# Optimization experiments

Hardware: AMD Instinct MI355X
Metric: run time of the kernel (lower is better)

## Reference

```python
import jax, jax.numpy as jnp
import numpy as np
from jax import lax

USER_NUM = 100000
COMP_NUM = 50000
ENTITY_NUM = USER_NUM + COMP_NUM + 2  # 150002
N_ACTIVE = USER_NUM + COMP_NUM        # 150000 valid graph nodes
REL_NUM = 200
D = 128
T = 12        # timesteps
E = 250000    # edges per timestep
S = 20000     # seed (LSTM-updated) nodes per timestep
B = 1024      # user batch
USER_ID_MAX = 99999


def setup_inputs() -> dict:
    key = jax.random.key(0)
    ks = jax.random.split(key, 16)
    ent_emb = jax.random.normal(ks[0], (ENTITY_NUM, D), jnp.float32) * 0.02
    c0_emb = jax.random.normal(ks[1], (ENTITY_NUM, D), jnp.float32) * 0.02
    rel_emb = jax.random.normal(ks[2], (REL_NUM, D), jnp.float32) * 0.02
    W_ih = jax.random.normal(ks[3], (4 * D, D), jnp.float32) * (1.0 / np.sqrt(D))
    W_hh = jax.random.normal(ks[4], (4 * D, D), jnp.float32) * (1.0 / np.sqrt(D))
    b_ih = jax.random.normal(ks[5], (4 * D,), jnp.float32) * 0.01
    b_hh = jax.random.normal(ks[6], (4 * D,), jnp.float32) * 0.01
    src = jax.random.randint(ks[7], (T, E), 0, N_ACTIVE, jnp.int32)
    dst = jax.random.randint(ks[8], (T, E), 0, N_ACTIVE, jnp.int32)
    rel_idx = jax.random.randint(ks[9], (T, E), 0, REL_NUM, jnp.int32)
    # unique seed nodes per timestep (scatter targets must not collide)
    seed_keys = jax.random.split(ks[10], T)
    seed_idx = jax.vmap(lambda k: jax.random.permutation(k, N_ACTIVE)[:S])(seed_keys).astype(jnp.int32)
    user_batch = jax.random.randint(ks[11], (B,), 0, USER_NUM, jnp.int32)
    comp_target = jax.random.randint(ks[12], (B,), 0, COMP_NUM, jnp.int32)
    job_target = jax.random.randint(ks[13], (B,), 0, REL_NUM // 2, jnp.int32)
    return {"ent_emb": ent_emb, "c0_emb": c0_emb, "rel_emb": rel_emb,
            "W_ih": W_ih, "W_hh": W_hh, "b_ih": b_ih, "b_hh": b_hh,
            "src": src, "dst": dst, "rel_idx": rel_idx, "seed_idx": seed_idx,
            "user_batch": user_batch, "comp_target": comp_target, "job_target": job_target}


def reference(ent_emb, c0_emb, rel_emb, W_ih, W_hh, b_ih, b_hh,
              src, dst, rel_idx, seed_idx, user_batch, comp_target, job_target):
    def step(carry, xs):
        h, c = carry                       # [N, D] node_emb / cx
        s, d, r, seed = xs
        # msg_GCN: m = src_node_emb * rel_emb[rel]; reduce_GCN: mean over mailbox
        m = h[s] * rel_emb[r]              # [E, D]
        msum = jax.ops.segment_sum(m, d, num_segments=ENTITY_NUM)
        cnt = jax.ops.segment_sum(jnp.ones((E,), h.dtype), d, num_segments=ENTITY_NUM)
        x = h + msum / jnp.maximum(cnt, 1.0)[:, None]   # update_node: node_emb + node_emb2
        # LSTMCell on seed nodes only (input = aggregated emb, state = pre-agg emb, cx)
        xi, hp, cp = x[seed], h[seed], c[seed]          # [S, D]
        gates = xi @ W_ih.T + b_ih + hp @ W_hh.T + b_hh  # [S, 4D]
        ig, fg, gg, og = jnp.split(gates, 4, axis=-1)
        cn = jax.nn.sigmoid(fg) * cp + jax.nn.sigmoid(ig) * jnp.tanh(gg)
        hn = jax.nn.sigmoid(og) * jnp.tanh(cn)
        return (x.at[seed].set(hn), c.at[seed].set(cn)), None

    (h, _c), _ = lax.scan(step, (ent_emb, c0_emb), (src, dst, rel_idx, seed_idx))

    u = h[user_batch]                                   # [B, D] user time embeddings
    # company softmax-CE (logsumexp over all companies)
    tc = ent_emb[comp_target + USER_ID_MAX + 1]
    all_c = ent_emb[USER_ID_MAX + 1: USER_ID_MAX + 1 + COMP_NUM]  # [COMP_NUM, D]
    pos_c = jnp.sum(u * tc, axis=1)
    comp_loss = -jnp.sum(pos_c - jax.nn.logsumexp(u @ all_c.T, axis=1))
    # job (relation) softmax-CE over rel_num // 2 jobs
    tj = rel_emb[job_target]
    all_j = rel_emb[: REL_NUM // 2]
    pos_j = jnp.sum(u * tj, axis=1)
    job_loss = -jnp.sum(pos_j - jax.nn.logsumexp(u @ all_j.T, axis=1))
    return jnp.stack([comp_loss, job_loss])
```

## Files before the change

kernel.cpp:

```cpp
#include <hip/hip_runtime.h>
#include <math.h>

typedef __attribute__((ext_vector_type(8))) short short8;
typedef __attribute__((ext_vector_type(8))) unsigned short u16x8;
typedef __attribute__((ext_vector_type(4))) float f32x4;

#define USER_NUM_  100000
#define COMP_NUM_  50000
#define EN         150002
#define REL_NUM_   200
#define DD         128
#define TT         12
#define EE         250000
#define SS         20000
#define BB         1024
#define NBLK       587
#define PPART      125
#define TILES_PP   25
#define NB         37
#define BSH        12
#define CHUNK      4096
#define NCH        62

__device__ inline unsigned short f2bf(float f) {
    unsigned u = __float_as_uint(f);
    unsigned r = (u + 0x7fffu + ((u >> 16) & 1u)) >> 16;
    return (unsigned short)r;
}

__device__ inline float bf2f(unsigned short u) {
    return __uint_as_float((unsigned)u << 16);
}

__device__ inline float sigmoidf_(float x) { return 1.f / (1.f + __expf(-x)); }

__device__ inline void lse_push(float v, float& m, float& s) {
    if (v <= m) { s += __expf(v - m); }
    else { s = s * __expf(m - v) + 1.f; m = v; }
}

__device__ inline void lse_merge(float& M, float& S, float M2, float S2) {
    float Mn = fmaxf(M, M2);
    S = S * __expf(M - Mn) + S2 * __expf(M2 - Mn);
    M = Mn;
}

__global__ __launch_bounds__(256) void packBF_k(const float* __restrict__ src, ushort4* __restrict__ dst, int n4) {
    int i = blockIdx.x * 256 + threadIdx.x;
    if (i >= n4) return;
    float4 v = ((const float4*)src)[i];
    ushort4 o;
    o.x = f2bf(v.x); o.y = f2bf(v.y); o.z = f2bf(v.z); o.w = f2bf(v.w);
    dst[i] = o;
}

__global__ __launch_bounds__(256) void zero_i32_k(int* __restrict__ p, int n) {
    int i = blockIdx.x * 256 + threadIdx.x;
    if (i < n) p[i] = 0;
}

__global__ __launch_bounds__(256) void prepW_k(const float* __restrict__ Wih, const float* __restrict__ Whh,
                                               const float* __restrict__ bih, const float* __restrict__ bhh,
                                               short* __restrict__ Wt, float* __restrict__ bsum) {
    int n = blockIdx.x;
    int k = threadIdx.x;
    float v = (k < 128) ? Wih[n * 128 + k] : Whh[n * 128 + (k - 128)];
    Wt[n * 256 + k] = (short)f2bf(v);
    if (k == 0) bsum[n] = bih[n] + bhh[n];
}

__global__ __launch_bounds__(256) void binA_k(const int* __restrict__ dst, int* __restrict__ bcnt,
                                              int t0) {
    int slot = blockIdx.y;
    int tid = threadIdx.x;
    int e = blockIdx.x * 256 + tid;
    __shared__ int lcnt[NB];
    if (tid < NB) lcnt[tid] = 0;
    __syncthreads();
    if (e < EE) {
        int d = __builtin_nontemporal_load(&dst[(size_t)(t0 + slot) * EE + e]);
        atomicAdd(&lcnt[d >> BSH], 1);
    }
    __syncthreads();
    if (tid < NB && lcnt[tid] > 0) atomicAdd(&bcnt[slot * NB + tid], lcnt[tid]);
}

__global__ __launch_bounds__(64) void binScan_k(const int* __restrict__ bcnt, int* __restrict__ bbase,
                                                int* __restrict__ bcur, int nt) {
    int slot = threadIdx.x;
    if (slot >= nt) return;
    int b = 0;
    for (int c = 0; c < NB; ++c) {
        bbase[slot * (NB + 1) + c] = b;
        bcur[slot * NB + c] = b;
        b += bcnt[slot * NB + c];
    }
    bbase[slot * (NB + 1) + NB] = b;
}

__global__ __launch_bounds__(256) void binB_k(const int* __restrict__ src, const int* __restrict__ dst,
                                              const int* __restrict__ rel, int* __restrict__ bcur,
                                              int2* __restrict__ bucketed, int t0) {
    int slot = blockIdx.y;
    int tid = threadIdx.x;
    int c0 = blockIdx.x * CHUNK;
    __shared__ int lcnt[NB], lbase[NB], gbase[NB], lcur[NB];
    __shared__ int2 stage[CHUNK];
    if (tid < NB) lcnt[tid] = 0;
    __syncthreads();

    int myb[16]; int2 myv[16];
#pragma unroll
    for (int i = 0; i < 16; ++i) {
        int e = c0 + i * 256 + tid;
        if (e < EE) {
            size_t gi = (size_t)(t0 + slot) * EE + e;
            int d = __builtin_nontemporal_load(&dst[gi]);
            int s = __builtin_nontemporal_load(&src[gi]);
            int r = __builtin_nontemporal_load(&rel[gi]);
            myb[i] = d >> BSH;
            myv[i] = make_int2(d, s | (r << 18));
            atomicAdd(&lcnt[myb[i]], 1);
        } else myb[i] = -1;
    }
    __syncthreads();
    if (tid == 0) {
        int b = 0;
        for (int c = 0; c < NB; ++c) { lbase[c] = b; b += lcnt[c]; }
    }
    __syncthreads();
    if (tid < NB) {
        gbase[tid] = (lcnt[tid] > 0) ? atomicAdd(&bcur[slot * NB + tid], lcnt[tid]) : 0;
        lcur[tid] = lbase[tid];
    }
    __syncthreads();
#pragma unroll
    for (int i = 0; i < 16; ++i) {
        if (myb[i] >= 0) {
            int p = atomicAdd(&lcur[myb[i]], 1);
            stage[p] = myv[i];
        }
    }
    __syncthreads();
    int w = tid >> 6, lane = tid & 63;
    int2* bout = bucketed + (size_t)slot * EE;
    for (int b = w; b < NB; b += 4) {
        int cnt = lcnt[b], lb = lbase[b], gb = gbase[b];
        for (int j = lane; j < cnt; j += 64)
            bout[gb + j] = stage[lb + j];
    }
}

__global__ __launch_bounds__(256) void histB_k(const int2* __restrict__ bucketed,
                                               const int* __restrict__ bbase,
                                               int* __restrict__ startp) {
    int b = blockIdx.x, slot = blockIdx.y;
    int tid = threadIdx.x;
    int base_ent = b << BSH;
    int nloc = EN - base_ent; if (nloc > 4096) nloc = 4096;
    __shared__ int lcnt[4096];
    for (int i = tid; i < nloc; i += 256) lcnt[i] = 0;
    __syncthreads();
    int e0 = bbase[slot * (NB + 1) + b], e1 = bbase[slot * (NB + 1) + b + 1];
    for (int e = e0 + tid; e < e1; e += 256) {
        int2 ed = bucketed[(size_t)slot * EE + e];
        atomicAdd(&lcnt[ed.x - base_ent], 1);
    }
    __syncthreads();
    for (int i = tid; i < nloc; i += 256) startp[(size_t)slot * EN + base_ent + i] = lcnt[i];
}

__global__ __launch_bounds__(256) void scanA_k(int* __restrict__ startp, int* __restrict__ bsums) {
    int slot = blockIdx.y;
    int tid = threadIdx.x;
    int i = blockIdx.x * 256 + tid;
    int v = (i < EN) ? startp[slot * EN + i] : 0;
    __shared__ int lds[256];
    lds[tid] = v; __syncthreads();
#pragma unroll
    for (int o = 1; o < 256; o <<= 1) {
        int x = (tid >= o) ? lds[tid - o] : 0;
        __syncthreads();
        lds[tid] += x;
        __syncthreads();
    }
    if (i < EN) startp[slot * EN + i] = lds[tid] - v;
    if (tid == 255) bsums[slot * NBLK + blockIdx.x] = lds[tid];
}

__global__ __launch_bounds__(1024) void scanB_k(int* __restrict__ bsums) {
    int slot = blockIdx.x;
    int tid = threadIdx.x;
    int v = (tid < NBLK) ? bsums[slot * NBLK + tid] : 0;
    __shared__ int lds[1024];
    lds[tid] = v; __syncthreads();
#pragma unroll
    for (int o = 1; o < 1024; o <<= 1) {
        int x = (tid >= o) ? lds[tid - o] : 0;
        __syncthreads();
        lds[tid] += x;
        __syncthreads();
    }
    if (tid < NBLK) bsums[slot * NBLK + tid] = lds[tid] - v;
}

__global__ __launch_bounds__(256) void scanC_k(int* __restrict__ startp, const int* __restrict__ bsums) {
    int slot = blockIdx.y;
    int i = blockIdx.x * 256 + threadIdx.x;
    if (i < EN) startp[slot * EN + i] += bsums[slot * NBLK + blockIdx.x];
}

__global__ __launch_bounds__(256) void scatB_k(const int2* __restrict__ bucketed,
                                               const int* __restrict__ bbase,
                                               int* __restrict__ startp, int* __restrict__ pairs) {
    int b = blockIdx.x, slot = blockIdx.y;
    int tid = threadIdx.x;
    int base_ent = b << BSH;
    int nloc = EN - base_ent; if (nloc > 4096) nloc = 4096;
    __shared__ int lcur[4096];
    for (int i = tid; i < nloc; i += 256) lcur[i] = startp[(size_t)slot * EN + base_ent + i];
    __syncthreads();
    int e0 = bbase[slot * (NB + 1) + b], e1 = bbase[slot * (NB + 1) + b + 1];
    for (int e = e0 + tid; e < e1; e += 256) {
        int2 ed = bucketed[(size_t)slot * EE + e];
        int pos = atomicAdd(&lcur[ed.x - base_ent], 1);
        pairs[(size_t)slot * EE + pos] = ed.y;
    }
    __syncthreads();
    for (int i = tid; i < nloc; i += 256) startp[(size_t)slot * EN + base_ent + i] = lcur[i];
}

__global__ __launch_bounds__(256) void agg_k(const unsigned short* __restrict__ hold,
                                             unsigned short* __restrict__ hnew,
                                             const unsigned short* __restrict__ Rbf,
                                             const int* __restrict__ endp_all,
                                             const int* __restrict__ pairs, int slot) {
    int tid = threadIdx.x;
    int d = blockIdx.x * 16 + (tid >> 4);
    int l = tid & 15;
    if (d >= EN) return;
    const int* endp = endp_all + (size_t)slot * EN;
    int e0 = (d > 0) ? endp[d - 1] : 0;
    int e1 = endp[d];
    const int* pp = pairs + (size_t)slot * EE;
    float acc[8];
#pragma unroll
    for (int j = 0; j < 8; ++j) acc[j] = 0.f;
    int e = e0;
    for (; e + 2 <= e1; e += 2) {
        int pk0 = pp[e], pk1 = pp[e + 1];
        u16x8 h0 = *(const u16x8*)(hold + (size_t)(pk0 & 0x3FFFF) * DD + l * 8);
        u16x8 r0 = *(const u16x8*)(Rbf + (size_t)(pk0 >> 18) * DD + l * 8);
        u16x8 h1 = *(const u16x8*)(hold + (size_t)(pk1 & 0x3FFFF) * DD + l * 8);
        u16x8 r1 = *(const u16x8*)(Rbf + (size_t)(pk1 >> 18) * DD + l * 8);
#pragma unroll
        for (int j = 0; j < 8; ++j)
            acc[j] = fmaf(bf2f(h1[j]), bf2f(r1[j]), fmaf(bf2f(h0[j]), bf2f(r0[j]), acc[j]));
    }
    if (e < e1) {
        int pk0 = pp[e];
        u16x8 h0 = *(const u16x8*)(hold + (size_t)(pk0 & 0x3FFFF) * DD + l * 8);
        u16x8 r0 = *(const u16x8*)(Rbf + (size_t)(pk0 >> 18) * DD + l * 8);
#pragma unroll
        for (int j = 0; j < 8; ++j)
            acc[j] = fmaf(bf2f(h0[j]), bf2f(r0[j]), acc[j]);
    }
    u16x8 hd = *(const u16x8*)(hold + (size_t)d * DD + l * 8);
    int c = e1 - e0;
    float inv = (c > 0) ? 1.f / (float)c : 0.f;
    u16x8 o;
#pragma unroll
    for (int j = 0; j < 8; ++j) o[j] = f2bf(fmaf(acc[j], inv, bf2f(hd[j])));
    *(u16x8*)(hnew + (size_t)d * DD + l * 8) = o;
}

__global__ __launch_bounds__(256) void lstm_k(const unsigned short* __restrict__ hold,
                                              unsigned short* __restrict__ hnew,
                                              unsigned short* __restrict__ cbuf, const short* __restrict__ Wt,
                                              const float* __restrict__ bsum, const int* __restrict__ seed) {
    int w = threadIdx.x >> 6;
    int lane = threadIdx.x & 63;
    int lrow = lane & 15, lhi = lane >> 4;
    int m0 = blockIdx.x * 32;
    int w32 = w * 32;

    const unsigned short* pxi[2];
    const unsigned short* php[2];
#pragma unroll
    for (int mi = 0; mi < 2; ++mi) {
        int m = m0 + mi * 16 + lrow;
        int sd = seed[m];
        pxi[mi] = hnew + (size_t)sd * DD;
        php[mi] = hold + (size_t)sd * DD;
    }

    f32x4 acc[2][4][2];
#pragma unroll
    for (int mi = 0; mi < 2; ++mi)
#pragma unroll
        for (int g = 0; g < 4; ++g)
#pragma unroll
            for (int s = 0; s < 2; ++s)
                acc[mi][g][s] = (f32x4){0.f, 0.f, 0.f, 0.f};

#pragma unroll
    for (int kk = 0; kk < 8; ++kk) {
        int klane = kk * 32 + lhi * 8;
        short8 af[2];
#pragma unroll
        for (int mi = 0; mi < 2; ++mi) {
            const unsigned short* p = (klane < 128) ? (pxi[mi] + klane) : (php[mi] + (klane - 128));
            af[mi] = *(const short8*)p;
        }
#pragma unroll
        for (int g = 0; g < 4; ++g)
#pragma unroll
            for (int s = 0; s < 2; ++s) {
                int col = g * 128 + w32 + s * 16 + lrow;
                short8 bf = *(const short8*)(Wt + col * 256 + klane);
                acc[0][g][s] = __builtin_amdgcn_mfma_f32_16x16x32_bf16(af[0], bf, acc[0][g][s], 0, 0, 0);
                acc[1][g][s] = __builtin_amdgcn_mfma_f32_16x16x32_bf16(af[1], bf, acc[1][g][s], 0, 0, 0);
            }
    }

    __syncthreads();

#pragma unroll
    for (int mi = 0; mi < 2; ++mi) {
#pragma unroll
        for (int r = 0; r < 4; ++r) {
            int m = m0 + mi * 16 + lhi * 4 + r;
            int sd = seed[m];
#pragma unroll
            for (int s = 0; s < 2; ++s) {
                int d = w32 + s * 16 + lrow;
                float ig = acc[mi][0][s][r] + bsum[d];
                float fg = acc[mi][1][s][r] + bsum[128 + d];
                float gg = acc[mi][2][s][r] + bsum[256 + d];
                float og = acc[mi][3][s][r] + bsum[384 + d];
                float cp = bf2f(cbuf[(size_t)sd * DD + d]);
                float cn = sigmoidf_(fg) * cp + sigmoidf_(ig) * tanhf(gg);
                float hn = sigmoidf_(og) * tanhf(cn);
                cbuf[(size_t)sd * DD + d] = f2bf(cn);
                hnew[(size_t)sd * DD + d] = f2bf(hn);
            }
        }
    }
}

__global__ __launch_bounds__(256) void packU_k(const unsigned short* __restrict__ hfin, const int* __restrict__ ub,
                                               short* __restrict__ Ubf) {
    int i = blockIdx.x * 256 + threadIdx.x;
    if (i >= BB * DD) return;
    int u = i >> 7, k = i & 127;
    Ubf[i] = (short)hfin[(size_t)ub[u] * DD + k];
}

__global__ __launch_bounds__(256) void comp_mfma_k(const short* __restrict__ Ubf, const short* __restrict__ Cbf,
                                                   float* __restrict__ partm, float* __restrict__ parts) {
    int w = threadIdx.x >> 6, lane = threadIdx.x & 63;
    int lrow = lane & 15, lhi = lane >> 4;
    int ubase = blockIdx.x * 128 + w * 32;
    int p = blockIdx.y;

    short8 a[2][4];
#pragma unroll
    for (int s2 = 0; s2 < 2; ++s2)
#pragma unroll
        for (int kc = 0; kc < 4; ++kc)
            a[s2][kc] = *(const short8*)(Ubf + (size_t)(ubase + s2 * 16 + lrow) * DD + kc * 32 + lhi * 8);

    float m[2][4], s[2][4];
#pragma unroll
    for (int s2 = 0; s2 < 2; ++s2)
#pragma unroll
        for (int r = 0; r < 4; ++r) { m[s2][r] = -1e30f; s[s2][r] = 0.f; }

    int c0 = p * TILES_PP * 16;
    for (int tile = 0; tile < TILES_PP; ++tile) {
        int comp = c0 + tile * 16 + lrow;
        f32x4 acc0 = {0.f, 0.f, 0.f, 0.f};
        f32x4 acc1 = {0.f, 0.f, 0.f, 0.f};
#pragma unroll
        for (int kc = 0; kc < 4; ++kc) {
            short8 b = *(const short8*)(Cbf + (size_t)comp * DD + kc * 32 + lhi * 8);
            acc0 = __builtin_amdgcn_mfma_f32_16x16x32_bf16(a[0][kc], b, acc0, 0, 0, 0);
            acc1 = __builtin_amdgcn_mfma_f32_16x16x32_bf16(a[1][kc], b, acc1, 0, 0, 0);
        }
#pragma unroll
        for (int r = 0; r < 4; ++r) {
            lse_push(acc0[r], m[0][r], s[0][r]);
            lse_push(acc1[r], m[1][r], s[1][r]);
        }
    }

#pragma unroll
    for (int s2 = 0; s2 < 2; ++s2)
#pragma unroll
        for (int r = 0; r < 4; ++r) {
            float M = m[s2][r], S = s[s2][r];
#pragma unroll
            for (int o = 1; o < 16; o <<= 1) {
                float M2 = __shfl_xor(M, o, 64);
                float S2 = __shfl_xor(S, o, 64);
                if (M2 > M) { S = S * __expf(M - M2) + S2; M = M2; }
                else { S += S2 * __expf(M2 - M); }
            }
            if (lrow == 0) {
                int u = ubase + s2 * 16 + lhi * 4 + r;
                partm[(size_t)u * PPART + p] = M;
                parts[(size_t)u * PPART + p] = S;
            }
        }
}

__global__ __launch_bounds__(256) void finish2_k(const unsigned short* __restrict__ hfin,
                                                 const float* __restrict__ ent,
                                                 const float* __restrict__ rel, const int* __restrict__ ub,
                                                 const int* __restrict__ ct, const int* __restrict__ jt,
                                                 const float* __restrict__ partm, const float* __restrict__ parts,
                                                 float* __restrict__ out) {
    __shared__ float s_u[4][128];
    int w = threadIdx.x >> 6, lane = threadIdx.x & 63;
    int u = blockIdx.x * 4 + w;

    const unsigned short* up = hfin + (size_t)ub[u] * DD;
    float u0 = bf2f(up[lane]), u1 = bf2f(up[lane + 64]);
    s_u[w][lane] = u0;
    s_u[w][lane + 64] = u1;

    const float* tcp = ent + (size_t)(USER_NUM_ + ct[u]) * DD;
    float pc = u0 * tcp[lane] + u1 * tcp[lane + 64];
    const float* tjp = rel + (size_t)jt[u] * DD;
    float pj = u0 * tjp[lane] + u1 * tjp[lane + 64];
#pragma unroll
    for (int o = 1; o < 64; o <<= 1) {
        pc += __shfl_xor(pc, o, 64);
        pj += __shfl_xor(pj, o, 64);
    }

    float M = partm[(size_t)u * PPART + lane];
    float S = parts[(size_t)u * PPART + lane];
    if (lane + 64 < PPART)
        lse_merge(M, S, partm[(size_t)u * PPART + lane + 64], parts[(size_t)u * PPART + lane + 64]);
#pragma unroll
    for (int o = 1; o < 64; o <<= 1) {
        float M2 = __shfl_xor(M, o, 64);
        float S2 = __shfl_xor(S, o, 64);
        lse_merge(M, S, M2, S2);
    }
    float lse_c = M + logf(S);

    int j1 = lane, j2 = lane + 64;
    bool v2 = j2 < (REL_NUM_ / 2);
    const float* r1 = rel + (size_t)j1 * DD;
    const float* r2 = rel + (size_t)(v2 ? j2 : 0) * DD;
    float d1 = 0.f, d2 = 0.f;
#pragma unroll 16
    for (int k = 0; k < DD; ++k) {
        float uk = s_u[w][k];
        d1 = fmaf(uk, r1[k], d1);
        d2 = fmaf(uk, r2[k], d2);
    }
    float Mj = d1, Sj = 1.f;
    if (v2) lse_push(d2, Mj, Sj);
#pragma unroll
    for (int o = 1; o < 64; o <<= 1) {
        float M2 = __shfl_xor(Mj, o, 64);
        float S2 = __shfl_xor(Sj, o, 64);
        lse_merge(Mj, Sj, M2, S2);
    }
    float lse_j = Mj + logf(Sj);

    if (lane == 0) {
        atomicAdd(&out[0], lse_c - pc);
        atomicAdd(&out[1], lse_j - pj);
    }
}

static inline size_t rup(size_t x) { return (x + 255) & ~(size_t)255; }

extern "C" void kernel_launch(void* const* d_in, const int* in_sizes, int n_in,
                              void* d_out, int out_size, void* d_ws, size_t ws_size,
                              hipStream_t stream) {
    const float* ent_emb = (const float*)d_in[0];
    const float* c0_emb  = (const float*)d_in[1];
    const float* rel_emb = (const float*)d_in[2];
    const float* W_ih    = (const float*)d_in[3];
    const float* W_hh    = (const float*)d_in[4];
    const float* b_ih    = (const float*)d_in[5];
    const float* b_hh    = (const float*)d_in[6];
    const int* src       = (const int*)d_in[7];
    const int* dst       = (const int*)d_in[8];
    const int* rel_idx   = (const int*)d_in[9];
    const int* seed_idx  = (const int*)d_in[10];
    const int* ubatch    = (const int*)d_in[11];
    const int* ctarg     = (const int*)d_in[12];
    const int* jtarg     = (const int*)d_in[13];
    float* out = (float*)d_out;

    const size_t HBH = (size_t)EN * DD * 2;

    char* base = (char*)d_ws;
    unsigned short* h0   = (unsigned short*)base;
    unsigned short* h1   = (unsigned short*)(base + HBH);
    unsigned short* cbuf = (unsigned short*)(base + 2 * HBH);

    int* startp; int* pairs; int* bsums; int2* bucketed; int* bcnt; int* bbase; int* bcur;
    short* Wt; float* bsumv; unsigned short* Rbf;
    auto place = [&](int NT) -> size_t {
        size_t o = 3 * HBH;
        startp   = (int*)(base + o);  o += rup((size_t)NT * EN * 4);
        pairs    = (int*)(base + o);  o += rup((size_t)NT * EE * 4);
        bucketed = (int2*)(base + o); o += rup((size_t)NT * EE * 8);
        bsums    = (int*)(base + o);  o += rup((size_t)NT * NBLK * 4);
        bcnt     = (int*)(base + o);  o += rup((size_t)NT * NB * 4);
        bbase    = (int*)(base + o);  o += rup((size_t)NT * (NB + 1) * 4);
        bcur     = (int*)(base + o);  o += rup((size_t)NT * NB * 4);
        Wt       = (short*)(base + o); o += rup(512 * 256 * 2);
        bsumv    = (float*)(base + o); o += rup(512 * 4);
        Rbf      = (unsigned short*)(base + o); o += rup((size_t)REL_NUM_ * DD * 2);
        return o;
    };

    const int cands[6] = {12, 6, 4, 3, 2, 1};
    int NT = 1;
    for (int i = 0; i < 6; ++i) {
        if (place(cands[i]) <= ws_size) { NT = cands[i]; break; }
    }
    place(NT);

    char* q = (char*)cbuf;
    short* Cbf = (short*)q;            q += rup((size_t)COMP_NUM_ * DD * 2);
    short* Ubf = (short*)q;            q += rup((size_t)BB * DD * 2);
    float* partm = (float*)q;          q += rup((size_t)BB * PPART * 4);
    float* parts = (float*)q;

    hipMemsetAsync(d_out, 0, 2 * sizeof(float), stream);

    const int n4 = EN * DD / 4;
    const int gcpy = (n4 + 255) / 256;
    const int ge = (EE + 255) / 256;

    prepW_k<<<512, 256, 0, stream>>>(W_ih, W_hh, b_ih, b_hh, Wt, bsumv);
    packBF_k<<<gcpy, 256, 0, stream>>>(ent_emb, (ushort4*)h0, n4);
    packBF_k<<<gcpy, 256, 0, stream>>>(c0_emb, (ushort4*)cbuf, n4);
    packBF_k<<<(REL_NUM_ * DD / 4 + 255) / 256, 256, 0, stream>>>(rel_emb, (ushort4*)Rbf, REL_NUM_ * DD / 4);

    auto build = [&](int t0, int nt) {
        zero_i32_k<<<(nt * NB + 255) / 256, 256, 0, stream>>>(bcnt, nt * NB);
        binA_k<<<dim3(ge, nt), 256, 0, stream>>>(dst, bcnt, t0);
        binScan_k<<<1, 64, 0, stream>>>(bcnt, bbase, bcur, nt);
        binB_k<<<dim3(NCH, nt), 256, 0, stream>>>(src, dst, rel_idx, bcur, bucketed, t0);
        histB_k<<<dim3(NB, nt), 256, 0, stream>>>(bucketed, bbase, startp);
        scanA_k<<<dim3(NBLK, nt), 256, 0, stream>>>(startp, bsums);
        scanB_k<<<nt, 1024, 0, stream>>>(bsums);
        scanC_k<<<dim3(NBLK, nt), 256, 0, stream>>>(startp, bsums);
        scatB_k<<<dim3(NB, nt), 256, 0, stream>>>(bucketed, bbase, startp, pairs);
    };

    unsigned short* hold = h0;
    unsigned short* hnew = h1;
    const int gagg = (EN + 15) / 16;

    for (int b0 = 0; b0 < TT; b0 += NT) {
        int nb = (TT - b0 < NT) ? (TT - b0) : NT;
        build(b0, nb);
        for (int k = 0; k < nb; ++k) {
            int t = b0 + k;
            agg_k<<<gagg, 256, 0, stream>>>(hold, hnew, Rbf, startp, pairs, k);
            lstm_k<<<SS / 32, 256, 0, stream>>>(hold, hnew, cbuf, Wt, bsumv, seed_idx + (size_t)t * SS);
            unsigned short* tmp = hold; hold = hnew; hnew = tmp;
        }
    }

    packBF_k<<<(COMP_NUM_ * DD / 4 + 255) / 256, 256, 0, stream>>>(ent_emb + (size_t)USER_NUM_ * DD,
                                                                   (ushort4*)Cbf, COMP_NUM_ * DD / 4);
    packU_k<<<(BB * DD + 255) / 256, 256, 0, stream>>>(hold, ubatch, Ubf);
    comp_mfma_k<<<dim3(BB / 128, PPART), 256, 0, stream>>>(Ubf, Cbf, partm, parts);
    finish2_k<<<BB / 4, 256, 0, stream>>>(hold, ent_emb, rel_emb, ubatch, ctarg, jtarg,
                                          partm, parts, out);
}
```

Measured before the change: 1.002 ms.

## Coarsen bin counting, stage company tiles in LDS, drop max-tracking in logsumexp

```diff
diff --git a/kernel.cpp b/kernel.cpp
--- a/kernel.cpp
+++ b/kernel.cpp
@@ -73,16 +73,22 @@
                                               int t0) {
     int slot = blockIdx.y;
     int tid = threadIdx.x;
-    int e = blockIdx.x * 256 + tid;
-    __shared__ int lcnt[NB];
-    if (tid < NB) lcnt[tid] = 0;
-    __syncthreads();
-    if (e < EE) {
-        int d = __builtin_nontemporal_load(&dst[(size_t)(t0 + slot) * EE + e]);
-        atomicAdd(&lcnt[d >> BSH], 1);
-    }
-    __syncthreads();
-    if (tid < NB && lcnt[tid] > 0) atomicAdd(&bcnt[slot * NB + tid], lcnt[tid]);
+    int c0 = blockIdx.x * CHUNK;
+    int w = tid >> 6;
+    __shared__ int lcnt[4][NB];
+    for (int i = tid; i < 4 * NB; i += 256) ((int*)lcnt)[i] = 0;
+    __syncthreads();
+#pragma unroll
+    for (int i = 0; i < 16; ++i) {
+        int e = c0 + i * 256 + tid;
+        if (e < EE) {
+            int d = __builtin_nontemporal_load(&dst[(size_t)(t0 + slot) * EE + e]);
+            atomicAdd(&lcnt[w][d >> BSH], 1);
+        }
+    }
+    __syncthreads();
+    if (tid < NB)
+        atomicAdd(&bcnt[slot * NB + tid], lcnt[0][tid] + lcnt[1][tid] + lcnt[2][tid] + lcnt[3][tid]);
 }
 
 __global__ __launch_bounds__(64) void binScan_k(const int* __restrict__ bcnt, int* __restrict__ bbase,
@@ -358,11 +364,14 @@
 
 __global__ __launch_bounds__(256) void comp_mfma_k(const short* __restrict__ Ubf, const short* __restrict__ Cbf,
                                                    float* __restrict__ partm, float* __restrict__ parts) {
-    int w = threadIdx.x >> 6, lane = threadIdx.x & 63;
+    int tid = threadIdx.x;
+    int w = tid >> 6, lane = tid & 63;
     int lrow = lane & 15, lhi = lane >> 4;
     int ubase = blockIdx.x * 128 + w * 32;
     int p = blockIdx.y;
 
+    __shared__ __align__(16) short ct[2][16][136];
+
     short8 a[2][4];
 #pragma unroll
     for (int s2 = 0; s2 < 2; ++s2)
@@ -370,27 +379,40 @@
         for (int kc = 0; kc < 4; ++kc)
             a[s2][kc] = *(const short8*)(Ubf + (size_t)(ubase + s2 * 16 + lrow) * DD + kc * 32 + lhi * 8);
 
-    float m[2][4], s[2][4];
+    float s[2][4];
 #pragma unroll
     for (int s2 = 0; s2 < 2; ++s2)
 #pragma unroll
-        for (int r = 0; r < 4; ++r) { m[s2][r] = -1e30f; s[s2][r] = 0.f; }
+        for (int r = 0; r < 4; ++r) s[s2][r] = 0.f;
 
     int c0 = p * TILES_PP * 16;
+    int srow = tid >> 4, scol = (tid & 15) * 8;
+    {
+        short8 v = *(const short8*)(Cbf + (size_t)(c0 + srow) * DD + scol);
+        *(short8*)&ct[0][srow][scol] = v;
+    }
+
     for (int tile = 0; tile < TILES_PP; ++tile) {
-        int comp = c0 + tile * 16 + lrow;
+        int cur = tile & 1;
+        short8 pf;
+        bool hn = (tile + 1 < TILES_PP);
+        if (hn)
+            pf = *(const short8*)(Cbf + (size_t)(c0 + (tile + 1) * 16 + srow) * DD + scol);
+        __syncthreads();
+        if (hn) *(short8*)&ct[cur ^ 1][srow][scol] = pf;
+
         f32x4 acc0 = {0.f, 0.f, 0.f, 0.f};
         f32x4 acc1 = {0.f, 0.f, 0.f, 0.f};
 #pragma unroll
         for (int kc = 0; kc < 4; ++kc) {
-            short8 b = *(const short8*)(Cbf + (size_t)comp * DD + kc * 32 + lhi * 8);
+            short8 b = *(const short8*)&ct[cur][lrow][kc * 32 + lhi * 8];
             acc0 = __builtin_amdgcn_mfma_f32_16x16x32_bf16(a[0][kc], b, acc0, 0, 0, 0);
             acc1 = __builtin_amdgcn_mfma_f32_16x16x32_bf16(a[1][kc], b, acc1, 0, 0, 0);
         }
 #pragma unroll
         for (int r = 0; r < 4; ++r) {
-            lse_push(acc0[r], m[0][r], s[0][r]);
-            lse_push(acc1[r], m[1][r], s[1][r]);
+            s[0][r] += __expf(acc0[r]);
+            s[1][r] += __expf(acc1[r]);
         }
     }
 
@@ -398,17 +420,13 @@
     for (int s2 = 0; s2 < 2; ++s2)
 #pragma unroll
         for (int r = 0; r < 4; ++r) {
-            float M = m[s2][r], S = s[s2][r];
-#pragma unroll
-            for (int o = 1; o < 16; o <<= 1) {
-                float M2 = __shfl_xor(M, o, 64);
-                float S2 = __shfl_xor(S, o, 64);
-                if (M2 > M) { S = S * __expf(M - M2) + S2; M = M2; }
-                else { S += S2 * __expf(M2 - M); }
-            }
+            float S = s[s2][r];
+#pragma unroll
+            for (int o = 1; o < 16; o <<= 1)
+                S += __shfl_xor(S, o, 64);
             if (lrow == 0) {
                 int u = ubase + s2 * 16 + lhi * 4 + r;
-                partm[(size_t)u * PPART + p] = M;
+                partm[(size_t)u * PPART + p] = 0.f;
                 parts[(size_t)u * PPART + p] = S;
             }
         }
@@ -540,7 +558,6 @@
 
     const int n4 = EN * DD / 4;
     const int gcpy = (n4 + 255) / 256;
-    const int ge = (EE + 255) / 256;
 
     prepW_k<<<512, 256, 0, stream>>>(W_ih, W_hh, b_ih, b_hh, Wt, bsumv);
     packBF_k<<<gcpy, 256, 0, stream>>>(ent_emb, (ushort4*)h0, n4);
@@ -549,7 +566,7 @@
 
     auto build = [&](int t0, int nt) {
         zero_i32_k<<<(nt * NB + 255) / 256, 256, 0, stream>>>(bcnt, nt * NB);
-        binA_k<<<dim3(ge, nt), 256, 0, stream>>>(dst, bcnt, t0);
+        binA_k<<<dim3(NCH, nt), 256, 0, stream>>>(dst, bcnt, t0);
         binScan_k<<<1, 64, 0, stream>>>(bcnt, bbase, bcur, nt);
         binB_k<<<dim3(NCH, nt), 256, 0, stream>>>(src, dst, rel_idx, bcur, bucketed, t0);
         histB_k<<<dim3(NB, nt), 256, 0, stream>>>(bucketed, bbase, startp);
```

Result: faster. 926.0 us (-7.6%).
